# Kernel tuning notes

Hardware: AMD Instinct MI355X
Metric: run time of the kernel (lower is better)

Reference implementation:

```python
import jax, jax.numpy as jnp
import numpy as np

B, T, D, VQ, L2, HID = 8, 2048, 768, 64, 12, 1024
K = 2 ** L2          # 4096 codebook entries
N_MID = 4            # condition_layer=6 -> 1 input + 4 middle + 1 output Linear, 5 BatchNorms
EPS_N = 1e-6
EPS_BN = 1e-5


def setup_inputs() -> dict:
    key = jax.random.key(0)
    ks = jax.random.split(key, 10)
    g = lambda i, shape, sc: jax.random.normal(ks[i], shape, jnp.float32) * sc
    return {
        "h_in": jax.random.normal(ks[0], (B, D, T), jnp.float32),
        "attn_mask": jax.random.randint(ks[1], (B, T), 0, 2, jnp.int32),
        "proj_w": g(2, (VQ, D), 0.02), "proj_b": jnp.zeros((VQ,), jnp.float32),
        "inv_w": g(3, (D, VQ), 0.02), "inv_b": jnp.zeros((D,), jnp.float32),
        "mlp_w_in": g(4, (HID, L2), 0.1), "mlp_b_in": jnp.zeros((HID,), jnp.float32),
        "mlp_w_mid": g(5, (N_MID, HID, HID), 0.03), "mlp_b_mid": jnp.zeros((N_MID, HID), jnp.float32),
        "mlp_w_out": g(6, (VQ, HID), 0.03), "mlp_b_out": jnp.zeros((VQ,), jnp.float32),
        "bn_gamma": jnp.ones((N_MID + 1, HID), jnp.float32),
        "bn_beta": jnp.zeros((N_MID + 1, HID), jnp.float32),
    }


def _bn(x, gamma, beta):
    # BatchNorm1d, training mode: batch mean / biased var over codebook rows
    m = x.mean(axis=0)
    v = x.var(axis=0)
    return (x - m) * jax.lax.rsqrt(v + EPS_BN) * gamma + beta


def _l2norm(x):
    return x / (jnp.linalg.norm(x, axis=-1, keepdims=True) + EPS_N)


def reference(h_in, attn_mask, proj_w, proj_b, inv_w, inv_b,
              mlp_w_in, mlp_b_in, mlp_w_mid, mlp_b_mid, mlp_w_out, mlp_b_out,
              bn_gamma, bn_beta):
    # --- codebook: binary vectors -> condition MLP (Linear+BN+ReLU x5, Linear) ---
    ints = jnp.arange(K)
    bits = ((ints[:, None] & (1 << jnp.arange(L2 - 1, -1, -1))) > 0).astype(jnp.float32)  # [K, L2]
    x = jax.nn.relu(_bn(bits @ mlp_w_in.T + mlp_b_in, bn_gamma[0], bn_beta[0]))
    for i in range(N_MID):
        x = jax.nn.relu(_bn(x @ mlp_w_mid[i].T + mlp_b_mid[i], bn_gamma[i + 1], bn_beta[i + 1]))
    embed = x @ mlp_w_out.T + mlp_b_out          # [K, VQ]
    embed = _l2norm(embed)                        # sphere=True

    # --- project hidden states: h_in [B,D,T] -> [B,T,VQ] ---
    h = jnp.einsum('bdt,vd->btv', h_in, proj_w) + proj_b
    h = _l2norm(h)

    # --- pairwise squared distances to codebook, argmax of -d (== softmax argmax) ---
    hf = h.reshape(-1, VQ)                                       # [B*T, VQ]
    d = (hf ** 2).sum(-1, keepdims=True) + (embed ** 2).sum(-1) - 2.0 * (hf @ embed.T)  # [B*T, K]
    code = jnp.argmax(-d, axis=-1)                               # [B*T]

    # --- masked gather/scatter quantization (eval path: hard codes) ---
    mask = (attn_mask == 1)                                      # [B, T]
    h_vq = embed[code].reshape(B, T, VQ) * mask[..., None].astype(h.dtype)
    quantized = jnp.einsum('btv,dv->btd', h_vq, inv_w) + inv_b   # proj_inv -> [B, T, D]
    vq_code = jnp.where(mask, code.reshape(B, T), 0)
    return quantized, vq_code
```

## Files before the change

kernel.cpp:

```cpp
#include <hip/hip_runtime.h>
#include <stddef.h>

#define BB   8
#define TT_  2048
#define DD   768
#define VQ_  64
#define L2C  12
#define HID_ 1024
#define KK   4096
#define NMID 4
#define NT   (BB*TT_)

typedef _Float16 h8v __attribute__((ext_vector_type(8)));
typedef float    f4v __attribute__((ext_vector_type(4)));

#define GL16(g, l) __builtin_amdgcn_global_load_lds( \
    (const __attribute__((address_space(1))) void*)(g), \
    (__attribute__((address_space(3))) void*)(l), 16, 0, 0)

__global__ __launch_bounds__(256) void k_mlp_in(const float* __restrict__ w_in,
                                                const float* __restrict__ b_in,
                                                float* __restrict__ X) {
    __shared__ float ws_[256 * 12];
    __shared__ float bs_[256];
    int tid = threadIdx.x;
    int h0  = blockIdx.x * 256;
    for (int i = tid; i < 256 * 12; i += 256) ws_[i] = w_in[h0 * 12 + i];
    bs_[tid] = b_in[h0 + tid];
    __syncthreads();
    float w[12];
#pragma unroll
    for (int l = 0; l < 12; l++) w[l] = ws_[tid * 12 + l];
    float bias = bs_[tid];
    int k0 = blockIdx.y * 16;
    for (int kk = 0; kk < 16; kk++) {
        int k = k0 + kk;
        float acc = bias;
#pragma unroll
        for (int l = 0; l < 12; l++)
            if ((k >> (11 - l)) & 1) acc += w[l];
        X[(size_t)k * HID_ + h0 + tid] = acc;
    }
}

__global__ __launch_bounds__(256) void k_bn_stats1(const float* __restrict__ Y,
                                                   float* __restrict__ part) {
    int b = blockIdx.x;
    int c = blockIdx.y * 256 + threadIdx.x;
    const float* src = Y + ((size_t)b << 6) * HID_ + c;
    float s = 0.f, q = 0.f;
    for (int r = 0; r < 64; r++) {
        float v = src[(size_t)r << 10];
        s += v; q += v * v;
    }
    part[((size_t)b << 10) + c] = s;
    part[65536 + ((size_t)b << 10) + c] = q;
}

__global__ __launch_bounds__(256) void k_bn_stats2(const float* __restrict__ part,
                                                   float* __restrict__ mv) {
    int c = blockIdx.x * 256 + threadIdx.x;
    float s = 0.f, q = 0.f;
    for (int b = 0; b < 64; b++) {
        s += part[((size_t)b << 10) + c];
        q += part[65536 + ((size_t)b << 10) + c];
    }
    float m = s * (1.f / KK);
    float v = q * (1.f / KK) - m * m;
    mv[c] = m; mv[HID_ + c] = v;
}

__global__ __launch_bounds__(256) void k_bn_apply_split(const float* __restrict__ Y,
                                                        const float* __restrict__ mv,
                                                        const float* __restrict__ gamma,
                                                        const float* __restrict__ beta,
                                                        _Float16* __restrict__ Xhi,
                                                        _Float16* __restrict__ Xlo) {
    int i = blockIdx.x * 256 + threadIdx.x;
    int c = (i << 2) & (HID_ - 1);
    float4 x = ((const float4*)Y)[i];
    float4 m = *(const float4*)(mv + c);
    float4 v = *(const float4*)(mv + HID_ + c);
    float4 g = *(const float4*)(gamma + c);
    float4 b = *(const float4*)(beta + c);
    float o[4];
    o[0] = fmaxf(0.f, (x.x - m.x) * (1.f / sqrtf(v.x + 1e-5f)) * g.x + b.x);
    o[1] = fmaxf(0.f, (x.y - m.y) * (1.f / sqrtf(v.y + 1e-5f)) * g.y + b.y);
    o[2] = fmaxf(0.f, (x.z - m.z) * (1.f / sqrtf(v.z + 1e-5f)) * g.z + b.z);
    o[3] = fmaxf(0.f, (x.w - m.w) * (1.f / sqrtf(v.w + 1e-5f)) * g.w + b.w);
    union { _Float16 h[4]; uint2 u; } uh, ul;
#pragma unroll
    for (int j = 0; j < 4; j++) {
        _Float16 h = (_Float16)o[j];
        uh.h[j] = h;
        ul.h[j] = (_Float16)(o[j] - (float)h);
    }
    *(uint2*)(Xhi + ((size_t)i << 2)) = uh.u;
    *(uint2*)(Xlo + ((size_t)i << 2)) = ul.u;
}

__global__ __launch_bounds__(256) void k_gemm_mfma3(const _Float16* __restrict__ Ahi,
                                                    const _Float16* __restrict__ Alo,
                                                    const _Float16* __restrict__ Whi,
                                                    const _Float16* __restrict__ Wlo,
                                                    const float* __restrict__ bias,
                                                    float* __restrict__ C) {
    __shared__ __attribute__((aligned(128))) char lds[4 * 32768];
    const int tid = threadIdx.x;
    const int wg = blockIdx.x;
    const int m0 = (wg & 31) << 7;
    const int n0 = (wg >> 5) << 7;
    const int wave = tid >> 6, lane = tid & 63;
    const int l15 = lane & 15, quad = lane >> 4;
    const int wm = (wave >> 1) << 6;
    const int wn = (wave & 1) << 6;

    const int rowA = (wave << 5) + (lane >> 2);
    const int colb = (lane & 3) << 4;
    const char* gA_h = (const char*)Ahi + ((size_t)(m0 + rowA) << 11) + colb;
    const char* gA_l = (const char*)Alo + ((size_t)(m0 + rowA) << 11) + colb;
    const char* gW_h = (const char*)Whi + ((size_t)(n0 + rowA) << 11) + colb;
    const char* gW_l = (const char*)Wlo + ((size_t)(n0 + rowA) << 11) + colb;
    const int dA = wave << 11;

    int offA[4], offW[4];
#pragma unroll
    for (int i = 0; i < 4; i++) offA[i] = ((wm + (i << 4) + l15) << 6) + (quad << 4);
#pragma unroll
    for (int j = 0; j < 4; j++) offW[j] = ((wn + (j << 4) + l15) << 6) + (quad << 4);

    f4v acc[4][4];
#pragma unroll
    for (int i = 0; i < 4; i++)
#pragma unroll
        for (int j = 0; j < 4; j++) acc[i][j] = (f4v){0.f, 0.f, 0.f, 0.f};

#define STG(bufi, tt) do { \
        char* b_ = lds + ((bufi) << 15); int o_ = (tt) << 6; \
        GL16(gA_h + o_,         b_ + dA); \
        GL16(gA_h + 32768 + o_, b_ + dA + 1024); \
        GL16(gA_l + o_,         b_ + 8192 + dA); \
        GL16(gA_l + 32768 + o_, b_ + 8192 + dA + 1024); \
        GL16(gW_h + o_,         b_ + 16384 + dA); \
        GL16(gW_h + 32768 + o_, b_ + 16384 + dA + 1024); \
        GL16(gW_l + o_,         b_ + 24576 + dA); \
        GL16(gW_l + 32768 + o_, b_ + 24576 + dA + 1024); \
    } while (0)

    STG(0, 0); STG(1, 1); STG(2, 2);
    for (int t = 0; t < 32; ++t) {
        if (t <= 29)      asm volatile("s_waitcnt vmcnt(16)" ::: "memory");
        else if (t == 30) asm volatile("s_waitcnt vmcnt(8)"  ::: "memory");
        else              asm volatile("s_waitcnt vmcnt(0)"  ::: "memory");
        __builtin_amdgcn_s_barrier();
        asm volatile("" ::: "memory");
        if (t + 3 < 32) STG((t + 3) & 3, t + 3);
        const char* b = lds + ((size_t)(t & 3) << 15);
        h8v ah[4], al[4];
#pragma unroll
        for (int i = 0; i < 4; i++) {
            ah[i] = *(const h8v*)(b + offA[i]);
            al[i] = *(const h8v*)(b + 8192 + offA[i]);
        }
        __builtin_amdgcn_s_setprio(1);
#pragma unroll
        for (int j = 0; j < 4; j++) {
            h8v bh = *(const h8v*)(b + 16384 + offW[j]);
            h8v bl = *(const h8v*)(b + 24576 + offW[j]);
#pragma unroll
            for (int i = 0; i < 4; i++) {
                acc[i][j] = __builtin_amdgcn_mfma_f32_16x16x32_f16(ah[i], bh, acc[i][j], 0, 0, 0);
                acc[i][j] = __builtin_amdgcn_mfma_f32_16x16x32_f16(ah[i], bl, acc[i][j], 0, 0, 0);
                acc[i][j] = __builtin_amdgcn_mfma_f32_16x16x32_f16(al[i], bh, acc[i][j], 0, 0, 0);
            }
        }
        __builtin_amdgcn_s_setprio(0);
        asm volatile("" ::: "memory");
    }
#undef STG

#pragma unroll
    for (int j = 0; j < 4; j++) {
        int col = n0 + wn + (j << 4) + l15;
        float bv = bias[col];
#pragma unroll
        for (int i = 0; i < 4; i++) {
            int row = m0 + wm + (i << 4) + (quad << 2);
#pragma unroll
            for (int r = 0; r < 4; r++)
                C[(size_t)(row + r) * HID_ + col] = acc[i][j][r] + bv;
        }
    }
}

__global__ __launch_bounds__(256) void k_gemm_mfma2(const _Float16* __restrict__ Ahi,
                                                    const _Float16* __restrict__ Alo,
                                                    const _Float16* __restrict__ Whi,
                                                    const _Float16* __restrict__ Wlo,
                                                    const float* __restrict__ bias,
                                                    float* __restrict__ C,
                                                    int M, int N, int Kd) {
    __shared__ __attribute__((aligned(128))) char lds[2][24576];
    const int tid = threadIdx.x;
    int wg = blockIdx.x;
    const int nwg = gridDim.x;
    wg = (wg & 7) * (nwg >> 3) + (wg >> 3);
    const int nx = M >> 7;
    const int m0 = (wg % nx) << 7;
    const int n0 = (wg / nx) << 6;
    const int wave = tid >> 6, lane = tid & 63;
    const int l15 = lane & 15, quad = lane >> 4;
    const int wm = (wave >> 1) << 6;
    const int wn = (wave & 1) << 5;

    const int pA0 = ((wave << 1) | 0) * 1024 + lane * 16;
    const int pA1 = ((wave << 1) | 1) * 1024 + lane * 16;
    const int pW  = wave * 1024 + lane * 16;
    const int qA0 = pA0 ^ (((pA0 >> 7) & 3) << 4);
    const int qA1 = pA1 ^ (((pA1 >> 7) & 3) << 4);
    const int qW  = pW  ^ (((pW  >> 7) & 3) << 4);
    const size_t krow = (size_t)Kd * 2;
    const char* gAh0 = (const char*)Ahi + (size_t)(m0 + (qA0 >> 6)) * krow + (qA0 & 63);
    const char* gAh1 = (const char*)Ahi + (size_t)(m0 + (qA1 >> 6)) * krow + (qA1 & 63);
    const char* gAl0 = (const char*)Alo + (size_t)(m0 + (qA0 >> 6)) * krow + (qA0 & 63);
    const char* gAl1 = (const char*)Alo + (size_t)(m0 + (qA1 >> 6)) * krow + (qA1 & 63);
    const char* gWh  = (const char*)Whi + (size_t)(n0 + (qW >> 6)) * krow + (qW & 63);
    const char* gWl  = (const char*)Wlo + (size_t)(n0 + (qW >> 6)) * krow + (qW & 63);
    const int dA0 = (wave << 1) * 1024;
    const int dA1 = dA0 + 1024;
    const int dW  = wave * 1024;

    int offA[4], offW[2];
#pragma unroll
    for (int i = 0; i < 4; i++) {
        int r = wm + (i << 4) + l15;
        offA[i] = r * 64 + ((quad ^ ((r >> 1) & 3)) << 4);
    }
#pragma unroll
    for (int j = 0; j < 2; j++) {
        int r = wn + (j << 4) + l15;
        offW[j] = r * 64 + ((quad ^ ((r >> 1) & 3)) << 4);
    }

    f4v acc[4][2];
#pragma unroll
    for (int i = 0; i < 4; i++)
#pragma unroll
        for (int j = 0; j < 2; j++) acc[i][j] = (f4v){0.f, 0.f, 0.f, 0.f};

#define STAGE(bufi, tt) do { \
        char* b_ = lds[bufi]; size_t o_ = (size_t)(tt) << 6; \
        GL16(gAh0 + o_, b_ + dA0); \
        GL16(gAh1 + o_, b_ + dA1); \
        GL16(gAl0 + o_, b_ + 8192 + dA0); \
        GL16(gAl1 + o_, b_ + 8192 + dA1); \
        GL16(gWh  + o_, b_ + 16384 + dW); \
        GL16(gWl  + o_, b_ + 20480 + dW); \
    } while (0)

    STAGE(0, 0);
    const int nt = Kd >> 5;
    for (int t = 0; t < nt; ++t) {
        const int cur = t & 1;
        if (t + 1 < nt) {
            STAGE(cur ^ 1, t + 1);
            asm volatile("s_waitcnt vmcnt(6)" ::: "memory");
        } else {
            asm volatile("s_waitcnt vmcnt(0)" ::: "memory");
        }
        __builtin_amdgcn_s_barrier();
        asm volatile("" ::: "memory");
        const char* b = lds[cur];
        h8v ah[4], al[4], bh[2], bl[2];
#pragma unroll
        for (int i = 0; i < 4; i++) {
            ah[i] = *(const h8v*)(b + offA[i]);
            al[i] = *(const h8v*)(b + 8192 + offA[i]);
        }
#pragma unroll
        for (int j = 0; j < 2; j++) {
            bh[j] = *(const h8v*)(b + 16384 + offW[j]);
            bl[j] = *(const h8v*)(b + 20480 + offW[j]);
        }
        __builtin_amdgcn_s_setprio(1);
#pragma unroll
        for (int i = 0; i < 4; i++)
#pragma unroll
            for (int j = 0; j < 2; j++) {
                acc[i][j] = __builtin_amdgcn_mfma_f32_16x16x32_f16(ah[i], bh[j], acc[i][j], 0, 0, 0);
                acc[i][j] = __builtin_amdgcn_mfma_f32_16x16x32_f16(ah[i], bl[j], acc[i][j], 0, 0, 0);
                acc[i][j] = __builtin_amdgcn_mfma_f32_16x16x32_f16(al[i], bh[j], acc[i][j], 0, 0, 0);
            }
        __builtin_amdgcn_s_setprio(0);
        asm volatile("" ::: "memory");
        __builtin_amdgcn_s_barrier();
    }
#undef STAGE

#pragma unroll
    for (int j = 0; j < 2; j++) {
        int col = n0 + wn + (j << 4) + l15;
        float bv = bias[col];
#pragma unroll
        for (int i = 0; i < 4; i++) {
            int row = m0 + wm + (i << 4) + (quad << 2);
#pragma unroll
            for (int r = 0; r < 4; r++)
                C[(size_t)(row + r) * N + col] = acc[i][j][r] + bv;
        }
    }
}

__global__ __launch_bounds__(256) void k_l2norm(float* __restrict__ E,
                                                float* __restrict__ eqh,
                                                _Float16* __restrict__ Ehi,
                                                _Float16* __restrict__ Elo) {
    int tid = threadIdx.x;
    int row = blockIdx.x * 4 + (tid >> 6);
    int v = tid & 63;
    size_t off = ((size_t)row << 6) + v;
    float x = E[off];
    float ss = x * x;
#pragma unroll
    for (int o = 32; o; o >>= 1) ss += __shfl_xor(ss, o, 64);
    float inv = 1.f / (sqrtf(ss) + 1e-6f);
    float xn = x * inv;
    E[off] = xn;
    _Float16 hh = (_Float16)xn;
    Ehi[off] = hh;
    Elo[off] = (_Float16)(xn - (float)hh);
    if (v == 0) eqh[row] = -0.5f * (ss * inv * inv);
}

__global__ __launch_bounds__(256) void k_wsplit_all(const float* __restrict__ w_mid,
                                                    const float* __restrict__ w_out,
                                                    const float* __restrict__ proj_w,
                                                    _Float16* __restrict__ Wmh,
                                                    _Float16* __restrict__ Wml,
                                                    _Float16* __restrict__ Woh,
                                                    _Float16* __restrict__ Wol,
                                                    _Float16* __restrict__ pwhi,
                                                    _Float16* __restrict__ pwlo) {
    int i = blockIdx.x * 256 + threadIdx.x;
    const float4* src; _Float16 *dh, *dl; int off;
    if (i < 1048576)            { src = (const float4*)w_mid;  dh = Wmh;  dl = Wml;  off = i; }
    else if (i < 1048576+16384) { src = (const float4*)w_out;  dh = Woh;  dl = Wol;  off = i - 1048576; }
    else                        { src = (const float4*)proj_w; dh = pwhi; dl = pwlo; off = i - 1048576 - 16384; }
    float4 w = src[off];
    float wf[4] = {w.x, w.y, w.z, w.w};
    union { _Float16 h[4]; uint2 u; } uh, ul;
#pragma unroll
    for (int j = 0; j < 4; j++) {
        _Float16 h = (_Float16)wf[j];
        uh.h[j] = h;
        ul.h[j] = (_Float16)(wf[j] - (float)h);
    }
    *(uint2*)(dh + ((size_t)off << 2)) = uh.u;
    *(uint2*)(dl + ((size_t)off << 2)) = ul.u;
}

__global__ __launch_bounds__(256) void k_cvt_inv(const float* __restrict__ iw,
                                                 _Float16* __restrict__ iwh) {
    int i = blockIdx.x * 256 + threadIdx.x;
    float4 w = ((const float4*)iw)[i];
    union { _Float16 h[4]; uint2 u; } uh;
    uh.h[0] = (_Float16)w.x; uh.h[1] = (_Float16)w.y;
    uh.h[2] = (_Float16)w.z; uh.h[3] = (_Float16)w.w;
    *(uint2*)(iwh + ((size_t)i << 2)) = uh.u;
}

__global__ __launch_bounds__(256) void k_proj_mfma(const float* __restrict__ h_in,
                                                   const _Float16* __restrict__ pwhi,
                                                   const _Float16* __restrict__ pwlo,
                                                   float* __restrict__ Hpart) {
    __shared__ float shA[128 * 33];
    const int tid = threadIdx.x;
    const int t0 = blockIdx.x * 128;
    const int ks = blockIdx.y;
    const int b = t0 >> 11;
    const int tloc0 = t0 & (TT_ - 1);
    const int wave = tid >> 6, lane = tid & 63;
    const int l15 = lane & 15, quad = lane >> 4;

    const int dl = tid >> 3;
    const int tg = (tid & 7) << 4;

    f4v acc[2][4];
#pragma unroll
    for (int i = 0; i < 2; i++)
#pragma unroll
        for (int j = 0; j < 4; j++) acc[i][j] = (f4v){0.f, 0.f, 0.f, 0.f};

    for (int kk = 0; kk < 6; kk++) {
        int dd0 = ks * 192 + kk * 32;
        const float* src = h_in + ((size_t)(b * DD + dd0 + dl) << 11) + tloc0 + tg;
        float4 g0 = *(const float4*)(src);
        float4 g1 = *(const float4*)(src + 4);
        float4 g2 = *(const float4*)(src + 8);
        float4 g3 = *(const float4*)(src + 12);
        __syncthreads();
        float gv[16] = {g0.x, g0.y, g0.z, g0.w, g1.x, g1.y, g1.z, g1.w,
                        g2.x, g2.y, g2.z, g2.w, g3.x, g3.y, g3.z, g3.w};
#pragma unroll
        for (int i = 0; i < 16; i++) shA[(tg + i) * 33 + dl] = gv[i];
        __syncthreads();

        h8v ah[2], al[2];
#pragma unroll
        for (int mt = 0; mt < 2; mt++) {
            const float* ap = &shA[((wave << 5) + (mt << 4) + l15) * 33 + (quad << 3)];
            float4 a0 = *(const float4*)(ap);
            float4 a1 = *(const float4*)(ap + 4);
            float av[8] = {a0.x, a0.y, a0.z, a0.w, a1.x, a1.y, a1.z, a1.w};
#pragma unroll
            for (int j = 0; j < 8; j++) {
                _Float16 h = (_Float16)av[j];
                ah[mt][j] = h;
                al[mt][j] = (_Float16)(av[j] - (float)h);
            }
        }
#pragma unroll
        for (int nt = 0; nt < 4; nt++) {
            size_t wb = (size_t)((nt << 4) + l15) * DD + dd0 + (quad << 3);
            h8v bh = *(const h8v*)(pwhi + wb);
            h8v bl = *(const h8v*)(pwlo + wb);
#pragma unroll
            for (int mt = 0; mt < 2; mt++) {
                acc[mt][nt] = __builtin_amdgcn_mfma_f32_16x16x32_f16(ah[mt], bh, acc[mt][nt], 0, 0, 0);
                acc[mt][nt] = __builtin_amdgcn_mfma_f32_16x16x32_f16(ah[mt], bl, acc[mt][nt], 0, 0, 0);
                acc[mt][nt] = __builtin_amdgcn_mfma_f32_16x16x32_f16(al[mt], bh, acc[mt][nt], 0, 0, 0);
            }
        }
    }
    float* dst = Hpart + ((size_t)ks << 20);
#pragma unroll
    for (int mt = 0; mt < 2; mt++) {
#pragma unroll
        for (int r = 0; r < 4; r++) {
            int t = t0 + (wave << 5) + (mt << 4) + (quad << 2) + r;
#pragma unroll
            for (int nt = 0; nt < 4; nt++)
                dst[((size_t)t << 6) + (nt << 4) + l15] = acc[mt][nt][r];
        }
    }
}

__global__ __launch_bounds__(256) void k_hnorm(const float* __restrict__ Hpart,
                                               const float* __restrict__ pb,
                                               _Float16* __restrict__ Hhi,
                                               _Float16* __restrict__ Hlo) {
    __shared__ float ssp[4][64];
    int tid = threadIdx.x;
    int tt = tid & 63, vg = tid >> 6;
    int t = blockIdx.x * 64 + tt;
    size_t base = ((size_t)t << 6) + (vg << 4);
    float o[16];
#pragma unroll
    for (int u = 0; u < 4; u++) {
        float4 p0 = *(const float4*)(Hpart + (0u << 20) + base + (u << 2));
        float4 p1 = *(const float4*)(Hpart + (1u << 20) + base + (u << 2));
        float4 p2 = *(const float4*)(Hpart + (2u << 20) + base + (u << 2));
        float4 p3 = *(const float4*)(Hpart + (3u << 20) + base + (u << 2));
        o[u * 4 + 0] = p0.x + p1.x + p2.x + p3.x;
        o[u * 4 + 1] = p0.y + p1.y + p2.y + p3.y;
        o[u * 4 + 2] = p0.z + p1.z + p2.z + p3.z;
        o[u * 4 + 3] = p0.w + p1.w + p2.w + p3.w;
    }
    float sp = 0.f;
#pragma unroll
    for (int j = 0; j < 16; j++) {
        o[j] += pb[(vg << 4) + j];
        sp = fmaf(o[j], o[j], sp);
    }
    ssp[vg][tt] = sp;
    __syncthreads();
    float ss = ssp[0][tt] + ssp[1][tt] + ssp[2][tt] + ssp[3][tt];
    float inv = 1.f / (sqrtf(ss) + 1e-6f);
    union { _Float16 h[8]; uint4 u; } uh0, uh1, ul0, ul1;
#pragma unroll
    for (int j = 0; j < 16; j++) {
        float xn = o[j] * inv;
        _Float16 hh = (_Float16)xn;
        _Float16 ll = (_Float16)(xn - (float)hh);
        if (j < 8) { uh0.h[j] = hh; ul0.h[j] = ll; }
        else       { uh1.h[j - 8] = hh; ul1.h[j - 8] = ll; }
    }
    *(uint4*)(Hhi + base)     = uh0.u;
    *(uint4*)(Hhi + base + 8) = uh1.u;
    *(uint4*)(Hlo + base)     = ul0.u;
    *(uint4*)(Hlo + base + 8) = ul1.u;
}

__global__ __launch_bounds__(256, 4) void k_argmax_mfma(const _Float16* __restrict__ Hhi,
                                                        const _Float16* __restrict__ Hlo,
                                                        const _Float16* __restrict__ Ehi,
                                                        const _Float16* __restrict__ Elo,
                                                        const float* __restrict__ eqh,
                                                        float* __restrict__ ps,
                                                        int* __restrict__ pi) {
    __shared__ __attribute__((aligned(128))) char elds[4 * 4096 + 1024];
    int tid = threadIdx.x;
    int wave = tid >> 6, lane = tid & 63;
    int l15 = lane & 15, quad = lane >> 4;
    int t0 = blockIdx.x * 256 + wave * 64;
    int kh = blockIdx.y;
    const int kbase = kh << 8;

    h8v hh0[4], hh1[4], hl0[4], hl1[4];
#pragma unroll
    for (int s = 0; s < 4; s++) {
        size_t hb = (size_t)(t0 + (s << 4) + l15) * 64 + (quad << 3);
        hh0[s] = *(const h8v*)(Hhi + hb);
        hh1[s] = *(const h8v*)(Hhi + hb + 32);
        hl0[s] = *(const h8v*)(Hlo + hb);
        hl1[s] = *(const h8v*)(Hlo + hb + 32);
    }
    float best[4] = {-1e30f, -1e30f, -1e30f, -1e30f};
    int   idx[4]  = {0, 0, 0, 0};

    const int p    = ((wave & 1) << 10) + lane * 16;
    const int srow = p >> 7;
    const int scol = (p & 127) ^ ((srow & 7) << 4);
    const char* gsrc0 = (const char*)((wave < 2) ? Ehi : Elo)
                      + (((size_t)kbase + srow) << 7) + scol;
    const int dwave = wave << 10;
#define ASTG(tt) GL16(gsrc0 + ((size_t)(tt) << 11), elds + (((tt) & 3) << 12) + dwave)

    const int rswz = (l15 & 7) << 4;
    const int o_e0 = l15 * 128 + ((quad << 4) ^ rswz);
    const int o_e1 = l15 * 128 + ((64 + (quad << 4)) ^ rswz);

    if (wave == 0) GL16((const char*)eqh + ((size_t)kbase << 2), elds + 16384);
    ASTG(0); ASTG(1); ASTG(2);

    for (int t = 0; t < 16; ++t) {
        if (t <= 13)      asm volatile("s_waitcnt vmcnt(2)" ::: "memory");
        else if (t == 14) asm volatile("s_waitcnt vmcnt(1)" ::: "memory");
        else              asm volatile("s_waitcnt vmcnt(0)" ::: "memory");
        __builtin_amdgcn_s_barrier();
        asm volatile("" ::: "memory");
        if (t + 3 < 16) ASTG(t + 3);
        const char* b = elds + ((size_t)(t & 3) << 12);
        h8v ce0 = *(const h8v*)(b + o_e0);
        h8v ce1 = *(const h8v*)(b + o_e1);
        h8v cl0 = *(const h8v*)(b + 2048 + o_e0);
        h8v cl1 = *(const h8v*)(b + 2048 + o_e1);
        float4 cq = *(const float4*)(elds + 16384 + (t << 6) + (quad << 4));
        int k0 = kbase + (t << 4);

        f4v acc[4];
#pragma unroll
        for (int s = 0; s < 4; s++) acc[s] = (f4v){0.f, 0.f, 0.f, 0.f};
        __builtin_amdgcn_s_setprio(1);
#pragma unroll
        for (int s = 0; s < 4; s++) acc[s] = __builtin_amdgcn_mfma_f32_16x16x32_f16(ce0, hh0[s], acc[s], 0, 0, 0);
#pragma unroll
        for (int s = 0; s < 4; s++) acc[s] = __builtin_amdgcn_mfma_f32_16x16x32_f16(ce1, hh1[s], acc[s], 0, 0, 0);
#pragma unroll
        for (int s = 0; s < 4; s++) acc[s] = __builtin_amdgcn_mfma_f32_16x16x32_f16(cl0, hh0[s], acc[s], 0, 0, 0);
#pragma unroll
        for (int s = 0; s < 4; s++) acc[s] = __builtin_amdgcn_mfma_f32_16x16x32_f16(cl1, hh1[s], acc[s], 0, 0, 0);
#pragma unroll
        for (int s = 0; s < 4; s++) acc[s] = __builtin_amdgcn_mfma_f32_16x16x32_f16(ce0, hl0[s], acc[s], 0, 0, 0);
#pragma unroll
        for (int s = 0; s < 4; s++) acc[s] = __builtin_amdgcn_mfma_f32_16x16x32_f16(ce1, hl1[s], acc[s], 0, 0, 0);
        __builtin_amdgcn_s_setprio(0);
        float qv[4] = {cq.x, cq.y, cq.z, cq.w};
#pragma unroll
        for (int r = 0; r < 4; r++) {
            int k = k0 + (quad << 2) + r;
#pragma unroll
            for (int s = 0; s < 4; s++) {
                float sc = acc[s][r] + qv[r];
                if (sc > best[s]) { best[s] = sc; idx[s] = k; }
            }
        }
        asm volatile("" ::: "memory");
    }
#undef ASTG

#pragma unroll
    for (int m = 16; m <= 32; m <<= 1) {
#pragma unroll
        for (int s = 0; s < 4; s++) {
            float ob = __shfl_xor(best[s], m, 64);
            int   oi = __shfl_xor(idx[s], m, 64);
            if (ob > best[s] || (ob == best[s] && oi < idx[s])) { best[s] = ob; idx[s] = oi; }
        }
    }
    if (quad == 0) {
#pragma unroll
        for (int s = 0; s < 4; s++) {
            int t = t0 + (s << 4) + l15;
            ps[(size_t)t * 16 + kh] = best[s];
            pi[(size_t)t * 16 + kh] = idx[s];
        }
    }
}

__global__ __launch_bounds__(256) void k_merge(const float* __restrict__ ps,
                                               const int* __restrict__ pi,
                                               const int* __restrict__ mask,
                                               const _Float16* __restrict__ Ehi,
                                               _Float16* __restrict__ G16,
                                               float* __restrict__ outc) {
    __shared__ int codes[256];
    __shared__ int ms[256];
    int tid = threadIdx.x;
    int base = blockIdx.x << 8;
    int t = base + tid;
    float best = ps[(size_t)t * 16];
    int bi = pi[(size_t)t * 16];
#pragma unroll
    for (int s = 1; s < 16; s++) {
        float v = ps[(size_t)t * 16 + s];
        if (v > best) { best = v; bi = pi[(size_t)t * 16 + s]; }
    }
    int m = mask[t];
    codes[tid] = bi;
    ms[tid] = m;
    outc[t] = m ? (float)bi : 0.0f;
    __syncthreads();
    for (int i = tid; i < 256 * 8; i += 256) {
        int r = i >> 3, u = i & 7;
        uint4 e = ms[r] ? ((const uint4*)(Ehi + ((size_t)codes[r] << 6)))[u]
                        : make_uint4(0u, 0u, 0u, 0u);
        ((uint4*)(G16 + ((size_t)(base + r) << 6)))[u] = e;
    }
}

__global__ __launch_bounds__(256) void k_gemm_out(const _Float16* __restrict__ G16,
                                                  const _Float16* __restrict__ iwh,
                                                  const float* __restrict__ bias,
                                                  float* __restrict__ C) {
    const int tid = threadIdx.x;
    const int t0 = blockIdx.x * 128, n0 = blockIdx.y * 64;
    const int wave = tid >> 6, lane = tid & 63;
    const int l15 = lane & 15, quad = lane >> 4;

    f4v acc[2][4];
#pragma unroll
    for (int i = 0; i < 2; i++)
#pragma unroll
        for (int j = 0; j < 4; j++) acc[i][j] = (f4v){0.f, 0.f, 0.f, 0.f};

#pragma unroll
    for (int ks = 0; ks < 2; ks++) {
        int kk = (ks << 5) + (quad << 3);
        h8v a[2], b[4];
#pragma unroll
        for (int mt = 0; mt < 2; mt++)
            a[mt] = *(const h8v*)(G16 + (size_t)(t0 + (wave << 5) + (mt << 4) + l15) * 64 + kk);
#pragma unroll
        for (int nt = 0; nt < 4; nt++)
            b[nt] = *(const h8v*)(iwh + (size_t)(n0 + (nt << 4) + l15) * 64 + kk);
#pragma unroll
        for (int mt = 0; mt < 2; mt++)
#pragma unroll
            for (int nt = 0; nt < 4; nt++)
                acc[mt][nt] = __builtin_amdgcn_mfma_f32_16x16x32_f16(a[mt], b[nt], acc[mt][nt], 0, 0, 0);
    }
#pragma unroll
    for (int nt = 0; nt < 4; nt++) {
        int col = n0 + (nt << 4) + l15;
        float bv = bias[col];
#pragma unroll
        for (int mt = 0; mt < 2; mt++) {
            int row = t0 + (wave << 5) + (mt << 4) + (quad << 2);
#pragma unroll
            for (int r = 0; r < 4; r++)
                C[(size_t)(row + r) * DD + col] = acc[mt][nt][r] + bv;
        }
    }
}

extern "C" void kernel_launch(void* const* d_in, const int* in_sizes, int n_in,
                              void* d_out, int out_size, void* d_ws, size_t ws_size,
                              hipStream_t stream) {
    const float* h_in   = (const float*)d_in[0];
    const int*   amask  = (const int*)d_in[1];
    const float* proj_w = (const float*)d_in[2];
    const float* proj_b = (const float*)d_in[3];
    const float* inv_w  = (const float*)d_in[4];
    const float* inv_b  = (const float*)d_in[5];
    const float* w_in   = (const float*)d_in[6];
    const float* b_in   = (const float*)d_in[7];
    const float* w_mid  = (const float*)d_in[8];
    const float* b_mid  = (const float*)d_in[9];
    const float* w_out  = (const float*)d_in[10];
    const float* b_out  = (const float*)d_in[11];
    const float* gamma  = (const float*)d_in[12];
    const float* beta   = (const float*)d_in[13];

    float*     Y    = (float*)d_ws;
    _Float16*  Xhi  = (_Float16*)(Y + (size_t)KK * HID_);
    _Float16*  Xlo  = Xhi + (size_t)KK * HID_;
    float*     mv   = (float*)(Xlo + (size_t)KK * HID_);
    float*     Emb  = mv + 2 * HID_;
    float*     eqh  = Emb + (size_t)KK * VQ_;
    float*     spart= eqh + KK;
    _Float16*  pwhi = (_Float16*)(spart + 2 * 65536);
    _Float16*  pwlo = pwhi + (size_t)VQ_ * DD;
    float*    Hpart = Y;
    _Float16* H16hi = Xhi;
    _Float16* H16lo = H16hi + (size_t)NT * VQ_;
    _Float16* E16hi = H16lo + (size_t)NT * VQ_;
    _Float16* E16lo = E16hi + (size_t)KK * VQ_;
    float*    ps    = (float*)(E16lo + (size_t)KK * VQ_);
    int*      pidx  = (int*)(ps + (size_t)NT * 16);
    _Float16* G16   = (_Float16*)(pidx + (size_t)NT * 16);
    _Float16* iwh   = G16 + (size_t)NT * VQ_;

    float* out_q = (float*)d_out;
    float* out_c = out_q + (size_t)NT * DD;

    _Float16* Wmh = (_Float16*)d_out;
    _Float16* Wml = Wmh + (size_t)NMID * HID_ * HID_;
    _Float16* Woh = Wml + (size_t)NMID * HID_ * HID_;
    _Float16* Wol = Woh + (size_t)VQ_ * HID_;

    k_wsplit_all<<<4208, 256, 0, stream>>>(w_mid, w_out, proj_w,
                                           Wmh, Wml, Woh, Wol, pwhi, pwlo);

    k_mlp_in<<<dim3(HID_ / 256, KK / 16), 256, 0, stream>>>(w_in, b_in, Y);
    k_bn_stats1<<<dim3(64, 4), 256, 0, stream>>>(Y, spart);
    k_bn_stats2<<<4, 256, 0, stream>>>(spart, mv);
    k_bn_apply_split<<<KK * HID_ / 1024, 256, 0, stream>>>(Y, mv, gamma, beta, Xhi, Xlo);
    for (int i = 0; i < NMID; i++) {
        k_gemm_mfma3<<<(KK / 128) * (HID_ / 128), 256, 0, stream>>>(
            Xhi, Xlo, Wmh + (size_t)i * HID_ * HID_, Wml + (size_t)i * HID_ * HID_,
            b_mid + (size_t)i * HID_, Y);
        k_bn_stats1<<<dim3(64, 4), 256, 0, stream>>>(Y, spart);
        k_bn_stats2<<<4, 256, 0, stream>>>(spart, mv);
        k_bn_apply_split<<<KK * HID_ / 1024, 256, 0, stream>>>(Y, mv,
            gamma + (size_t)(i + 1) * HID_, beta + (size_t)(i + 1) * HID_, Xhi, Xlo);
    }
    k_gemm_mfma2<<<(KK / 128) * (VQ_ / 64), 256, 0, stream>>>(
        Xhi, Xlo, Woh, Wol, b_out, Emb, KK, VQ_, HID_);
    k_l2norm<<<KK / 4, 256, 0, stream>>>(Emb, eqh, E16hi, E16lo);

    k_cvt_inv<<<VQ_ * DD / 1024, 256, 0, stream>>>(inv_w, iwh);
    k_proj_mfma<<<dim3(NT / 128, 4), 256, 0, stream>>>(h_in, pwhi, pwlo, Hpart);
    k_hnorm<<<NT / 64, 256, 0, stream>>>(Hpart, proj_b, H16hi, H16lo);
    k_argmax_mfma<<<dim3(NT / 256, 16), 256, 0, stream>>>(
        H16hi, H16lo, E16hi, E16lo, eqh, ps, pidx);
    k_merge<<<NT / 256, 256, 0, stream>>>(ps, pidx, amask, E16hi, G16, out_c);
    k_gemm_out<<<dim3(NT / 128, DD / 64), 256, 0, stream>>>(G16, iwh, inv_b, out_q);
}
```

Measured before the change: 453.3 us.

## Double-buffer LDS fragment reads in register to overlap with MFMA in mid GEMM

Restructures the k_gemm_mfma3 main loop into a ping-pong schedule. The LDS fragment reads for tile t+1 go into a second register set while the MFMAs for tile t run, and the loop is unrolled by two with explicit prologue and epilogue. Global-to-LDS staging moves one stage further ahead. Launch bounds now state one block per SM so the doubled fragment registers fit, at the cost of possible spills or lower occupancy.

```diff
diff --git a/kernel.cpp b/kernel.cpp
--- a/kernel.cpp
+++ b/kernel.cpp
@@ -99,12 +99,12 @@
     *(uint2*)(Xlo + ((size_t)i << 2)) = ul.u;
 }
 
-__global__ __launch_bounds__(256) void k_gemm_mfma3(const _Float16* __restrict__ Ahi,
-                                                    const _Float16* __restrict__ Alo,
-                                                    const _Float16* __restrict__ Whi,
-                                                    const _Float16* __restrict__ Wlo,
-                                                    const float* __restrict__ bias,
-                                                    float* __restrict__ C) {
+__global__ __launch_bounds__(256, 1) void k_gemm_mfma3(const _Float16* __restrict__ Ahi,
+                                                       const _Float16* __restrict__ Alo,
+                                                       const _Float16* __restrict__ Whi,
+                                                       const _Float16* __restrict__ Wlo,
+                                                       const float* __restrict__ bias,
+                                                       float* __restrict__ C) {
     __shared__ __attribute__((aligned(128))) char lds[4 * 32768];
     const int tid = threadIdx.x;
     const int wg = blockIdx.x;
@@ -134,6 +134,9 @@
     for (int i = 0; i < 4; i++)
 #pragma unroll
         for (int j = 0; j < 4; j++) acc[i][j] = (f4v){0.f, 0.f, 0.f, 0.f};
+
+    h8v aAh[4], aAl[4], wAh[4], wAl[4];
+    h8v aBh[4], aBl[4], wBh[4], wBl[4];
 
 #define STG(bufi, tt) do { \
         char* b_ = lds + ((bufi) << 15); int o_ = (tt) << 6; \
@@ -147,36 +150,84 @@
         GL16(gW_l + 32768 + o_, b_ + 24576 + dA + 1024); \
     } while (0)
 
+#define RD(tt, ah_, al_, bh_, bl_) do { \
+        const char* b_ = lds + ((size_t)((tt) & 3) << 15); \
+        _Pragma("unroll") \
+        for (int i = 0; i < 4; i++) { \
+            ah_[i] = *(const h8v*)(b_ + offA[i]); \
+            al_[i] = *(const h8v*)(b_ + 8192 + offA[i]); \
+        } \
+        _Pragma("unroll") \
+        for (int j = 0; j < 4; j++) { \
+            bh_[j] = *(const h8v*)(b_ + 16384 + offW[j]); \
+            bl_[j] = *(const h8v*)(b_ + 24576 + offW[j]); \
+        } \
+    } while (0)
+
+#define MM(ah_, al_, bh_, bl_) do { \
+        __builtin_amdgcn_s_setprio(1); \
+        _Pragma("unroll") \
+        for (int j = 0; j < 4; j++) \
+        _Pragma("unroll") \
+            for (int i = 0; i < 4; i++) { \
+                acc[i][j] = __builtin_amdgcn_mfma_f32_16x16x32_f16(ah_[i], bh_[j], acc[i][j], 0, 0, 0); \
+                acc[i][j] = __builtin_amdgcn_mfma_f32_16x16x32_f16(ah_[i], bl_[j], acc[i][j], 0, 0, 0); \
+                acc[i][j] = __builtin_amdgcn_mfma_f32_16x16x32_f16(al_[i], bh_[j], acc[i][j], 0, 0, 0); \
+            } \
+        __builtin_amdgcn_s_setprio(0); \
+    } while (0)
+
     STG(0, 0); STG(1, 1); STG(2, 2);
-    for (int t = 0; t < 32; ++t) {
-        if (t <= 29)      asm volatile("s_waitcnt vmcnt(16)" ::: "memory");
-        else if (t == 30) asm volatile("s_waitcnt vmcnt(8)"  ::: "memory");
-        else              asm volatile("s_waitcnt vmcnt(0)"  ::: "memory");
+    asm volatile("s_waitcnt vmcnt(16)" ::: "memory");
+    __builtin_amdgcn_s_barrier();
+    asm volatile("" ::: "memory");
+    STG(3, 3);
+    RD(0, aAh, aAl, wAh, wAl);
+
+    for (int p = 0; p < 14; ++p) {
+        const int t = 2 * p;
+        asm volatile("s_waitcnt vmcnt(16)" ::: "memory");
+        asm volatile("s_waitcnt lgkmcnt(0)" ::: "memory");
         __builtin_amdgcn_s_barrier();
         asm volatile("" ::: "memory");
-        if (t + 3 < 32) STG((t + 3) & 3, t + 3);
-        const char* b = lds + ((size_t)(t & 3) << 15);
-        h8v ah[4], al[4];
-#pragma unroll
-        for (int i = 0; i < 4; i++) {
-            ah[i] = *(const h8v*)(b + offA[i]);
-            al[i] = *(const h8v*)(b + 8192 + offA[i]);
-        }
-        __builtin_amdgcn_s_setprio(1);
-#pragma unroll
-        for (int j = 0; j < 4; j++) {
-            h8v bh = *(const h8v*)(b + 16384 + offW[j]);
-            h8v bl = *(const h8v*)(b + 24576 + offW[j]);
-#pragma unroll
-            for (int i = 0; i < 4; i++) {
-                acc[i][j] = __builtin_amdgcn_mfma_f32_16x16x32_f16(ah[i], bh, acc[i][j], 0, 0, 0);
-                acc[i][j] = __builtin_amdgcn_mfma_f32_16x16x32_f16(ah[i], bl, acc[i][j], 0, 0, 0);
-                acc[i][j] = __builtin_amdgcn_mfma_f32_16x16x32_f16(al[i], bh, acc[i][j], 0, 0, 0);
-            }
-        }
-        __builtin_amdgcn_s_setprio(0);
+        STG((t + 4) & 3, t + 4);
+        RD(t + 1, aBh, aBl, wBh, wBl);
+        MM(aAh, aAl, wAh, wAl);
         asm volatile("" ::: "memory");
-    }
+        asm volatile("s_waitcnt vmcnt(16)" ::: "memory");
+        asm volatile("s_waitcnt lgkmcnt(0)" ::: "memory");
+        __builtin_amdgcn_s_barrier();
+        asm volatile("" ::: "memory");
+        STG((t + 5) & 3, t + 5);
+        RD(t + 2, aAh, aAl, wAh, wAl);
+        MM(aBh, aBl, wBh, wBl);
+        asm volatile("" ::: "memory");
+    }
+    asm volatile("s_waitcnt vmcnt(16)" ::: "memory");
+    asm volatile("s_waitcnt lgkmcnt(0)" ::: "memory");
+    __builtin_amdgcn_s_barrier();
+    asm volatile("" ::: "memory");
+    RD(29, aBh, aBl, wBh, wBl);
+    MM(aAh, aAl, wAh, wAl);
+    asm volatile("" ::: "memory");
+    asm volatile("s_waitcnt vmcnt(8)" ::: "memory");
+    asm volatile("s_waitcnt lgkmcnt(0)" ::: "memory");
+    __builtin_amdgcn_s_barrier();
+    asm volatile("" ::: "memory");
+    RD(30, aAh, aAl, wAh, wAl);
+    MM(aBh, aBl, wBh, wBl);
+    asm volatile("" ::: "memory");
+    asm volatile("s_waitcnt vmcnt(0)" ::: "memory");
+    asm volatile("s_waitcnt lgkmcnt(0)" ::: "memory");
+    __builtin_amdgcn_s_barrier();
+    asm volatile("" ::: "memory");
+    RD(31, aBh, aBl, wBh, wBl);
+    MM(aAh, aAl, wAh, wAl);
+    asm volatile("" ::: "memory");
+    asm volatile("s_waitcnt lgkmcnt(0)" ::: "memory");
+    MM(aBh, aBl, wBh, wBl);
+#undef MM
+#undef RD
 #undef STG
 
 #pragma unroll
```

Result: no change. 455.1 us (+0.4%).
